# Kernel tuning notes

Hardware: AMD Instinct MI355X
Metric: run time of the kernel (lower is better)

The kernel has to match this reference:

```python
import jax, jax.numpy as jnp
import numpy as np

B, S, D, H, OPS = 1024, 512, 128, 128, 16
V2 = 64000  # vocabulary_size * 2


def _lstm_last(emb, lengths, W_ih, W_hh, b_ih, b_hh, h0, c0):
    # emb: [B, S, D]; returns hidden state at step lengths-1 for each sample: [B, H]
    bsz = emb.shape[0]
    x = jnp.swapaxes(emb, 0, 1)  # [S, B, D]
    h = jnp.broadcast_to(h0[0], (bsz, h0.shape[-1]))  # learnable init state, expanded over batch
    c = jnp.broadcast_to(c0[0], (bsz, c0.shape[-1]))

    def step(carry, x_t):
        h, c = carry
        gates = x_t @ W_ih.T + b_ih + h @ W_hh.T + b_hh  # [B, 4H]
        i, f, g, o = jnp.split(gates, 4, axis=-1)  # torch LSTM gate order: i, f, g, o
        i = jax.nn.sigmoid(i); f = jax.nn.sigmoid(f)
        g = jnp.tanh(g); o = jax.nn.sigmoid(o)
        c = f * c + i * g
        h = o * jnp.tanh(c)
        return (h, c), h

    _, hs = jax.lax.scan(step, (h, c), x)  # hs: [S, B, H]
    t = jnp.maximum(lengths, 1) - 1  # last valid step per ragged sequence
    return hs[t, jnp.arange(bsz)]  # [B, H]


def setup_inputs() -> dict:
    key = jax.random.key(0)
    ks = jax.random.split(key, 12)
    sc = 0.05
    return {
        "tokens": jax.random.randint(ks[0], (B, S), 0, V2, dtype=jnp.int32),
        "lengths": jax.random.randint(ks[1], (B,), 1, S + 1, dtype=jnp.int32),
        "operator_onehot": jax.random.uniform(ks[2], (B, OPS), dtype=jnp.float32),
        "embedding": jax.random.normal(ks[3], (V2, D), dtype=jnp.float32) * sc,
        "W_ih": jax.random.normal(ks[4], (4 * H, D), dtype=jnp.float32) * sc,
        "W_hh": jax.random.normal(ks[5], (4 * H, H), dtype=jnp.float32) * sc,
        "b_ih": jax.random.normal(ks[6], (4 * H,), dtype=jnp.float32) * sc,
        "b_hh": jax.random.normal(ks[7], (4 * H,), dtype=jnp.float32) * sc,
        "h0": jnp.zeros((1, 1, H), dtype=jnp.float32),
        "c0": jnp.zeros((1, 1, H), dtype=jnp.float32),
        "lin_W": jax.random.normal(ks[8], (2, H + OPS), dtype=jnp.float32) * sc,
        "lin_b": jax.random.normal(ks[9], (2,), dtype=jnp.float32) * sc,
    }


def reference(tokens, lengths, operator_onehot, embedding, W_ih, W_hh, b_ih, b_hh, h0, c0, lin_W, lin_b):
    emb = jax.nn.relu(embedding[tokens])  # [B, S, D] embedding lookup + ReLU
    h_last = jax.nn.relu(_lstm_last(emb, lengths, W_ih, W_hh, b_ih, b_hh, h0, c0))  # [B, H]
    combined = jnp.concatenate([h_last, operator_onehot], axis=1)  # feature union
    return combined @ lin_W.T + lin_b  # [B, 2] logits (training mode: no sigmoid)
```

## Files before the change

### kernel.cpp

```cpp
#include <hip/hip_runtime.h>
#include <hip/hip_bf16.h>

#define NB    1024
#define SEQ   512
#define DIM   128
#define HID   128
#define NOPS  16
#define FEAT  144
#define BQ    4
#define AST   144
#define XST   578
#define TKST  (SEQ + 16)

typedef __bf16 bf16x8 __attribute__((ext_vector_type(8)));
typedef float  floatx4 __attribute__((ext_vector_type(4)));

__device__ __forceinline__ float gate_s(float aL, float aH, float ka) {
    const float kS = -1.4426950408889634f;
    const float arg = __builtin_fmaf(kS, aL, __builtin_fmaf(kS, aH, ka));
    return __builtin_amdgcn_rcpf(1.0f + __builtin_amdgcn_exp2f(arg));
}
__device__ __forceinline__ float gate_t(float aL, float aH, float ka) {
    const float kT = -2.8853900817779268f;
    const float arg = __builtin_fmaf(kT, aL, __builtin_fmaf(kT, aH, ka));
    return 2.0f * __builtin_amdgcn_rcpf(1.0f + __builtin_amdgcn_exp2f(arg)) - 1.0f;
}
__device__ __forceinline__ float tanh_c(float x) {
    const float kT = -2.8853900817779268f;
    return 2.0f * __builtin_amdgcn_rcpf(1.0f + __builtin_amdgcn_exp2f(kT * x)) - 1.0f;
}

__device__ __forceinline__ void block_sync_lds() {
    asm volatile("s_waitcnt lgkmcnt(0)\n\ts_barrier" ::: "memory");
}

__global__ __launch_bounds__(512, 2)
void lstm_fused(const int* __restrict__ tokens, const int* __restrict__ lengths,
                const float* __restrict__ onehot, const float* __restrict__ emb,
                const float* __restrict__ Wih, const float* __restrict__ Whh,
                const float* __restrict__ bih, const float* __restrict__ bhh,
                const float* __restrict__ h0, const float* __restrict__ c0,
                const float* __restrict__ linW, const float* __restrict__ linb,
                float* __restrict__ out)
{
    __shared__ __align__(16) __bf16 xbuf[8 * XST];
    __shared__ __align__(16) __bf16 hbuf[2 * BQ * AST];
    __shared__ __align__(16) float  hlbuf[BQ * HID];
    __shared__ __align__(16) int    tkbuf[BQ * TKST];

    const int tid  = threadIdx.x;
    const int wave = tid >> 6;
    const int lane = tid & 63;
    const int quad = lane >> 4;
    const int lrow = lane & 15;
    const int bid  = blockIdx.x;

    bf16x8 wfx[4][4], wfh[4][4];
#pragma unroll
    for (int gt = 0; gt < 4; ++gt) {
        const int g = gt * 128 + wave * 16 + lrow;
#pragma unroll
        for (int kt = 0; kt < 4; ++kt) {
            const float* sx = Wih + g * DIM + kt * 32 + quad * 8;
            const float* sh = Whh + g * HID + kt * 32 + quad * 8;
            float4 a = *(const float4*)(sx);
            float4 b = *(const float4*)(sx + 4);
            bf16x8 v;
            v[0] = (__bf16)a.x; v[1] = (__bf16)a.y; v[2] = (__bf16)a.z; v[3] = (__bf16)a.w;
            v[4] = (__bf16)b.x; v[5] = (__bf16)b.y; v[6] = (__bf16)b.z; v[7] = (__bf16)b.w;
            wfx[gt][kt] = v;
            a = *(const float4*)(sh);
            b = *(const float4*)(sh + 4);
            v[0] = (__bf16)a.x; v[1] = (__bf16)a.y; v[2] = (__bf16)a.z; v[3] = (__bf16)a.w;
            v[4] = (__bf16)b.x; v[5] = (__bf16)b.y; v[6] = (__bf16)b.z; v[7] = (__bf16)b.w;
            wfh[gt][kt] = v;
        }
    }

    const int uu = wave * 16 + lrow;
    const int bq = bid * BQ + quad;
    int lenq = lengths[bq]; if (lenq < 1) lenq = 1;
    const int tlast = lenq - 1;

    int Lmax = 0;
#pragma unroll
    for (int s2 = 0; s2 < BQ; ++s2) {
        int l2 = lengths[bid * BQ + s2]; if (l2 < 1) l2 = 1;
        Lmax = (l2 > Lmax) ? l2 : Lmax;
    }

    const float kS = -1.4426950408889634f;
    const float kT = -2.8853900817779268f;
    const float karg0 = kS * (bih[0 * 128 + uu] + bhh[0 * 128 + uu]);
    const float karg1 = kS * (bih[1 * 128 + uu] + bhh[1 * 128 + uu]);
    const float karg2 = kT * (bih[2 * 128 + uu] + bhh[2 * 128 + uu]);
    const float karg3 = kS * (bih[3 * 128 + uu] + bhh[3 * 128 + uu]);

    float c  = c0[uu];
    float hl = 0.0f;

    const int m  = tid >> 7;
    const int u  = tid & 127;
    const int bm = bid * BQ + m;
    const int sm = m * AST + u;

    {
        const int4 tv = *(const int4*)(tokens + (size_t)bm * SEQ + (tid & 127) * 4);
        *(int4*)(&tkbuf[m * TKST + (tid & 127) * 4]) = tv;
        if (tid < BQ * 16)
            tkbuf[(tid >> 4) * TKST + SEQ + (tid & 15)] = 0;
    }

    hbuf[sm] = (__bf16)h0[u];
    const int* tokm = tokens + (size_t)bm * SEQ;
#pragma unroll
    for (int k = 0; k < 8; ++k) {
        float ek = emb[(size_t)tokm[k] * DIM + u];
        xbuf[k * XST + sm] = (__bf16)fmaxf(ek, 0.0f);
    }
    float e0 = emb[(size_t)tokm[8]  * DIM + u];
    float e1 = emb[(size_t)tokm[9]  * DIM + u];
    float e2 = emb[(size_t)tokm[10] * DIM + u];
    float e3 = emb[(size_t)tokm[11] * DIM + u];
    int   tk = tokm[12];

#define EREG(OFF) ((OFF) == 0 ? e0 : (OFF) == 1 ? e1 : (OFF) == 2 ? e2 : e3)

    const int xfbase = (lrow & 3) * XST + (lrow >> 2) * AST + quad * 8;
    const __bf16* const xfp[2] = { &xbuf[xfbase], &xbuf[4 * XST + xfbase] };
    const int habase = (lrow >> 2) * AST + quad * 8;
    const __bf16* const hf[2] = { &hbuf[habase], &hbuf[BQ * AST + habase] };
    __bf16* const hw[2] = { &hbuf[quad * AST + uu], &hbuf[BQ * AST + quad * AST + uu] };
    __bf16* const xw = &xbuf[sm];

    __syncthreads();

    const floatx4 zc = {0.0f, 0.0f, 0.0f, 0.0f};

    floatx4 xga[4], xgb[4];
    {
        bf16x8 af_[4];
#pragma unroll
        for (int kt = 0; kt < 4; ++kt)
            af_[kt] = *(const bf16x8*)(xfp[0] + kt * 32);
#pragma unroll
        for (int gt = 0; gt < 4; ++gt)
            xga[gt] = __builtin_amdgcn_mfma_f32_16x16x32_bf16(af_[0], wfx[gt][0], zc, 0, 0, 0);
#pragma unroll
        for (int kt = 1; kt < 4; ++kt)
#pragma unroll
            for (int gt = 0; gt < 4; ++gt)
                xga[gt] = __builtin_amdgcn_mfma_f32_16x16x32_bf16(af_[kt], wfx[gt][kt], xga[gt], 0, 0, 0);
    }
    block_sync_lds();

#define STEP(G, OFF, XGC, XGN) do {                                                  \
        const int t  = ts + OFF;                                                     \
        bf16x8 ah0 = *(const bf16x8*)(hf[OFF & 1] + 0 * 32);                         \
        bf16x8 ah2 = *(const bf16x8*)(hf[OFF & 1] + 2 * 32);                         \
        bf16x8 ah1 = *(const bf16x8*)(hf[OFF & 1] + 1 * 32);                         \
        bf16x8 ah3 = *(const bf16x8*)(hf[OFF & 1] + 3 * 32);                         \
        bf16x8 ax_ = *(const bf16x8*)(xfp[1 - (G)] + (OFF) * 32);                    \
        if (t + 8 < SEQ)         \
            xw[(4 * (G) + (OFF)) * XST] = (__bf16)fmaxf(EREG(OFF), 0.0f);            \
        if (t + 12 < SEQ)                                    \
            EREG(OFF) = emb[(size_t)tk * DIM + u];                                   \
        tk = tkbuf[m * TKST + t + 13];                                               \
        floatx4 aL[4], aH[4];                                                        \
        _Pragma("unroll") for (int gt = 0; gt < 4; ++gt)                             \
            aL[gt] = __builtin_amdgcn_mfma_f32_16x16x32_bf16(ah0, wfh[gt][0], XGC[gt], 0, 0, 0); \
        _Pragma("unroll") for (int gt = 0; gt < 4; ++gt)                             \
            aH[gt] = __builtin_amdgcn_mfma_f32_16x16x32_bf16(ah2, wfh[gt][2], zc, 0, 0, 0); \
        _Pragma("unroll") for (int gt = 0; gt < 4; ++gt)                             \
            aL[gt] = __builtin_amdgcn_mfma_f32_16x16x32_bf16(ah1, wfh[gt][1], aL[gt], 0, 0, 0); \
        _Pragma("unroll") for (int gt = 0; gt < 4; ++gt)                             \
            aH[gt] = __builtin_amdgcn_mfma_f32_16x16x32_bf16(ah3, wfh[gt][3], aH[gt], 0, 0, 0); \
        if (OFF == 0) {                                                              \
            _Pragma("unroll") for (int gt = 0; gt < 4; ++gt)                         \
                XGN[gt] = __builtin_amdgcn_mfma_f32_16x16x32_bf16(ax_, wfx[gt][0], zc, 0, 0, 0); \
        } else {                                                                     \
            _Pragma("unroll") for (int gt = 0; gt < 4; ++gt)                         \
                XGN[gt] = __builtin_amdgcn_mfma_f32_16x16x32_bf16(ax_, wfx[gt][OFF], XGN[gt], 0, 0, 0); \
        }                                                                            \
        const float ii = gate_s(aL[0][OFF], aH[0][OFF], karg0);                      \
        const float ff = gate_s(aL[1][OFF], aH[1][OFF], karg1);                      \
        const float g2 = gate_t(aL[2][OFF], aH[2][OFF], karg2);                      \
        const float oo = gate_s(aL[3][OFF], aH[3][OFF], karg3);                      \
        c = ff * c + ii * g2;                                                        \
        const float h = oo * tanh_c(c);                                              \
        if (t == tlast) hl = fmaxf(h, 0.0f);                                         \
        *hw[1 - (OFF & 1)] = (__bf16)h;                                              \
        block_sync_lds();                                                            \
    } while (0)

    for (int ts8 = 0; ts8 < Lmax; ts8 += 8) {
        {
            const int ts = ts8;
            STEP(0, 0, xga, xgb); STEP(0, 1, xga, xgb);
            STEP(0, 2, xga, xgb); STEP(0, 3, xga, xgb);
        }
        {
            const int ts = ts8 + 4;
            STEP(1, 0, xgb, xga); STEP(1, 1, xgb, xga);
            STEP(1, 2, xgb, xga); STEP(1, 3, xgb, xga);
        }
    }
#undef STEP
#undef EREG

    hlbuf[quad * HID + uu] = hl;
    __syncthreads();
    if (tid < 2 * BQ) {
        const int mm = tid >> 1, kk = tid & 1;
        const int bb = bid * BQ + mm;
        float a2 = linb[kk];
        for (int q = 0; q < HID; ++q)
            a2 += hlbuf[mm * HID + q] * linW[kk * FEAT + q];
        for (int o = 0; o < NOPS; ++o)
            a2 += onehot[bb * NOPS + o] * linW[kk * FEAT + HID + o];
        out[bb * 2 + kk] = a2;
    }
}

extern "C" void kernel_launch(void* const* d_in, const int* in_sizes, int n_in,
                              void* d_out, int out_size, void* d_ws, size_t ws_size,
                              hipStream_t stream) {
    const int*   tokens  = (const int*)d_in[0];
    const int*   lengths = (const int*)d_in[1];
    const float* onehot  = (const float*)d_in[2];
    const float* emb     = (const float*)d_in[3];
    const float* Wih     = (const float*)d_in[4];
    const float* Whh     = (const float*)d_in[5];
    const float* bih     = (const float*)d_in[6];
    const float* bhh     = (const float*)d_in[7];
    const float* h0      = (const float*)d_in[8];
    const float* c0      = (const float*)d_in[9];
    const float* linW    = (const float*)d_in[10];
    const float* linb    = (const float*)d_in[11];
    float* out = (float*)d_out;
    (void)in_sizes; (void)n_in; (void)out_size; (void)d_ws; (void)ws_size;

    lstm_fused<<<dim3(NB / BQ), dim3(512), 0, stream>>>(
        tokens, lengths, onehot, emb, Wih, Whh, bih, bhh, h0, c0, linW, linb, out);
}
```

Before: 421.8 us.

## Halve block to 4 waves, each owning two hidden-unit column tiles

The block drops from 512 to 256 threads, so each wave handles 32 hidden units (two 16-column MFMA tiles) instead of 16. Each wave holds twice the weight fragments in registers. The split-K aL/aH accumulation becomes a single 4-deep chain per tile. The input projection for the next 4 steps is now computed in one batch at step 3, instead of being spread over the steps. The aim is cheaper per-step barriers with fewer waves and more MFMA work between syncs. In exchange, register pressure rises, occupancy falls (launch bounds 256,1), and the per-step dependency chain gets longer.

```diff
diff --git a/kernel.cpp b/kernel.cpp
--- a/kernel.cpp
+++ b/kernel.cpp
@@ -15,15 +15,13 @@
 typedef __bf16 bf16x8 __attribute__((ext_vector_type(8)));
 typedef float  floatx4 __attribute__((ext_vector_type(4)));
 
-__device__ __forceinline__ float gate_s(float aL, float aH, float ka) {
+__device__ __forceinline__ float sig_a(float a, float ka) {
     const float kS = -1.4426950408889634f;
-    const float arg = __builtin_fmaf(kS, aL, __builtin_fmaf(kS, aH, ka));
-    return __builtin_amdgcn_rcpf(1.0f + __builtin_amdgcn_exp2f(arg));
-}
-__device__ __forceinline__ float gate_t(float aL, float aH, float ka) {
+    return __builtin_amdgcn_rcpf(1.0f + __builtin_amdgcn_exp2f(__builtin_fmaf(kS, a, ka)));
+}
+__device__ __forceinline__ float tanh_a(float a, float ka) {
     const float kT = -2.8853900817779268f;
-    const float arg = __builtin_fmaf(kT, aL, __builtin_fmaf(kT, aH, ka));
-    return 2.0f * __builtin_amdgcn_rcpf(1.0f + __builtin_amdgcn_exp2f(arg)) - 1.0f;
+    return 2.0f * __builtin_amdgcn_rcpf(1.0f + __builtin_amdgcn_exp2f(__builtin_fmaf(kT, a, ka))) - 1.0f;
 }
 __device__ __forceinline__ float tanh_c(float x) {
     const float kT = -2.8853900817779268f;
@@ -34,7 +32,7 @@
     asm volatile("s_waitcnt lgkmcnt(0)\n\ts_barrier" ::: "memory");
 }
 
-__global__ __launch_bounds__(512, 2)
+__global__ __launch_bounds__(256, 1)
 void lstm_fused(const int* __restrict__ tokens, const int* __restrict__ lengths,
                 const float* __restrict__ onehot, const float* __restrict__ emb,
                 const float* __restrict__ Wih, const float* __restrict__ Whh,
@@ -55,31 +53,34 @@
     const int lrow = lane & 15;
     const int bid  = blockIdx.x;
 
-    bf16x8 wfx[4][4], wfh[4][4];
+    bf16x8 wfx[4][2][4], wfh[4][2][4];
 #pragma unroll
     for (int gt = 0; gt < 4; ++gt) {
-        const int g = gt * 128 + wave * 16 + lrow;
-#pragma unroll
-        for (int kt = 0; kt < 4; ++kt) {
-            const float* sx = Wih + g * DIM + kt * 32 + quad * 8;
-            const float* sh = Whh + g * HID + kt * 32 + quad * 8;
-            float4 a = *(const float4*)(sx);
-            float4 b = *(const float4*)(sx + 4);
-            bf16x8 v;
-            v[0] = (__bf16)a.x; v[1] = (__bf16)a.y; v[2] = (__bf16)a.z; v[3] = (__bf16)a.w;
-            v[4] = (__bf16)b.x; v[5] = (__bf16)b.y; v[6] = (__bf16)b.z; v[7] = (__bf16)b.w;
-            wfx[gt][kt] = v;
-            a = *(const float4*)(sh);
-            b = *(const float4*)(sh + 4);
-            v[0] = (__bf16)a.x; v[1] = (__bf16)a.y; v[2] = (__bf16)a.z; v[3] = (__bf16)a.w;
-            v[4] = (__bf16)b.x; v[5] = (__bf16)b.y; v[6] = (__bf16)b.z; v[7] = (__bf16)b.w;
-            wfh[gt][kt] = v;
+#pragma unroll
+        for (int ct = 0; ct < 2; ++ct) {
+            const int g = gt * 128 + wave * 32 + ct * 16 + lrow;
+#pragma unroll
+            for (int kt = 0; kt < 4; ++kt) {
+                const float* sx = Wih + g * DIM + kt * 32 + quad * 8;
+                const float* sh = Whh + g * HID + kt * 32 + quad * 8;
+                float4 a = *(const float4*)(sx);
+                float4 b = *(const float4*)(sx + 4);
+                bf16x8 v;
+                v[0] = (__bf16)a.x; v[1] = (__bf16)a.y; v[2] = (__bf16)a.z; v[3] = (__bf16)a.w;
+                v[4] = (__bf16)b.x; v[5] = (__bf16)b.y; v[6] = (__bf16)b.z; v[7] = (__bf16)b.w;
+                wfx[gt][ct][kt] = v;
+                a = *(const float4*)(sh);
+                b = *(const float4*)(sh + 4);
+                v[0] = (__bf16)a.x; v[1] = (__bf16)a.y; v[2] = (__bf16)a.z; v[3] = (__bf16)a.w;
+                v[4] = (__bf16)b.x; v[5] = (__bf16)b.y; v[6] = (__bf16)b.z; v[7] = (__bf16)b.w;
+                wfh[gt][ct][kt] = v;
+            }
         }
     }
 
-    const int uu = wave * 16 + lrow;
-    const int bq = bid * BQ + quad;
-    int lenq = lengths[bq]; if (lenq < 1) lenq = 1;
+    const int uA = wave * 32 + lrow;
+    const int uB = uA + 16;
+    int lenq = lengths[bid * BQ + quad]; if (lenq < 1) lenq = 1;
     const int tlast = lenq - 1;
 
     int Lmax = 0;
@@ -91,124 +92,140 @@
 
     const float kS = -1.4426950408889634f;
     const float kT = -2.8853900817779268f;
-    const float karg0 = kS * (bih[0 * 128 + uu] + bhh[0 * 128 + uu]);
-    const float karg1 = kS * (bih[1 * 128 + uu] + bhh[1 * 128 + uu]);
-    const float karg2 = kT * (bih[2 * 128 + uu] + bhh[2 * 128 + uu]);
-    const float karg3 = kS * (bih[3 * 128 + uu] + bhh[3 * 128 + uu]);
-
-    float c  = c0[uu];
-    float hl = 0.0f;
-
-    const int m  = tid >> 7;
-    const int u  = tid & 127;
-    const int bm = bid * BQ + m;
-    const int sm = m * AST + u;
+    const float kA0 = kS * (bih[0 * 128 + uA] + bhh[0 * 128 + uA]);
+    const float kA1 = kS * (bih[1 * 128 + uA] + bhh[1 * 128 + uA]);
+    const float kA2 = kT * (bih[2 * 128 + uA] + bhh[2 * 128 + uA]);
+    const float kA3 = kS * (bih[3 * 128 + uA] + bhh[3 * 128 + uA]);
+    const float kB0 = kS * (bih[0 * 128 + uB] + bhh[0 * 128 + uB]);
+    const float kB1 = kS * (bih[1 * 128 + uB] + bhh[1 * 128 + uB]);
+    const float kB2 = kT * (bih[2 * 128 + uB] + bhh[2 * 128 + uB]);
+    const float kB3 = kS * (bih[3 * 128 + uB] + bhh[3 * 128 + uB]);
+
+    float cA = c0[uA], cB = c0[uB];
+    float hlA = 0.0f, hlB = 0.0f;
+
+    const int bm = bid * BQ + wave;
+    const int* tokm = tokens + (size_t)bm * SEQ;
 
     {
-        const int4 tv = *(const int4*)(tokens + (size_t)bm * SEQ + (tid & 127) * 4);
-        *(int4*)(&tkbuf[m * TKST + (tid & 127) * 4]) = tv;
+        *(int4*)(&tkbuf[wave * TKST + lane * 8])     = *(const int4*)(tokm + lane * 8);
+        *(int4*)(&tkbuf[wave * TKST + lane * 8 + 4]) = *(const int4*)(tokm + lane * 8 + 4);
         if (tid < BQ * 16)
             tkbuf[(tid >> 4) * TKST + SEQ + (tid & 15)] = 0;
     }
 
-    hbuf[sm] = (__bf16)h0[u];
-    const int* tokm = tokens + (size_t)bm * SEQ;
+    hbuf[wave * AST + lane]      = (__bf16)h0[lane];
+    hbuf[wave * AST + lane + 64] = (__bf16)h0[lane + 64];
 #pragma unroll
     for (int k = 0; k < 8; ++k) {
-        float ek = emb[(size_t)tokm[k] * DIM + u];
-        xbuf[k * XST + sm] = (__bf16)fmaxf(ek, 0.0f);
-    }
-    float e0 = emb[(size_t)tokm[8]  * DIM + u];
-    float e1 = emb[(size_t)tokm[9]  * DIM + u];
-    float e2 = emb[(size_t)tokm[10] * DIM + u];
-    float e3 = emb[(size_t)tokm[11] * DIM + u];
-    int   tk = tokm[12];
-
-#define EREG(OFF) ((OFF) == 0 ? e0 : (OFF) == 1 ? e1 : (OFF) == 2 ? e2 : e3)
+        const size_t row = (size_t)tokm[k] * DIM;
+        xbuf[k * XST + wave * AST + lane]      = (__bf16)fmaxf(emb[row + lane], 0.0f);
+        xbuf[k * XST + wave * AST + lane + 64] = (__bf16)fmaxf(emb[row + lane + 64], 0.0f);
+    }
+    float eA0 = emb[(size_t)tokm[8]  * DIM + lane], eB0 = emb[(size_t)tokm[8]  * DIM + lane + 64];
+    float eA1 = emb[(size_t)tokm[9]  * DIM + lane], eB1 = emb[(size_t)tokm[9]  * DIM + lane + 64];
+    float eA2 = emb[(size_t)tokm[10] * DIM + lane], eB2 = emb[(size_t)tokm[10] * DIM + lane + 64];
+    float eA3 = emb[(size_t)tokm[11] * DIM + lane], eB3 = emb[(size_t)tokm[11] * DIM + lane + 64];
+    int   tk  = tokm[12];
+
+#define EA(OFF) ((OFF) == 0 ? eA0 : (OFF) == 1 ? eA1 : (OFF) == 2 ? eA2 : eA3)
+#define EB(OFF) ((OFF) == 0 ? eB0 : (OFF) == 1 ? eB1 : (OFF) == 2 ? eB2 : eB3)
 
     const int xfbase = (lrow & 3) * XST + (lrow >> 2) * AST + quad * 8;
     const __bf16* const xfp[2] = { &xbuf[xfbase], &xbuf[4 * XST + xfbase] };
     const int habase = (lrow >> 2) * AST + quad * 8;
     const __bf16* const hf[2] = { &hbuf[habase], &hbuf[BQ * AST + habase] };
-    __bf16* const hw[2] = { &hbuf[quad * AST + uu], &hbuf[BQ * AST + quad * AST + uu] };
-    __bf16* const xw = &xbuf[sm];
+    __bf16* const hwA[2] = { &hbuf[quad * AST + uA], &hbuf[BQ * AST + quad * AST + uA] };
+    __bf16* const hwB[2] = { &hbuf[quad * AST + uB], &hbuf[BQ * AST + quad * AST + uB] };
+    __bf16* const xwA = &xbuf[wave * AST + lane];
+    __bf16* const xwB = &xbuf[wave * AST + lane + 64];
 
     __syncthreads();
 
     const floatx4 zc = {0.0f, 0.0f, 0.0f, 0.0f};
 
-    floatx4 xga[4], xgb[4];
+    floatx4 xg[4][2];
     {
         bf16x8 af_[4];
 #pragma unroll
         for (int kt = 0; kt < 4; ++kt)
             af_[kt] = *(const bf16x8*)(xfp[0] + kt * 32);
 #pragma unroll
-        for (int gt = 0; gt < 4; ++gt)
-            xga[gt] = __builtin_amdgcn_mfma_f32_16x16x32_bf16(af_[0], wfx[gt][0], zc, 0, 0, 0);
-#pragma unroll
-        for (int kt = 1; kt < 4; ++kt)
+        for (int kt = 0; kt < 4; ++kt)
 #pragma unroll
             for (int gt = 0; gt < 4; ++gt)
-                xga[gt] = __builtin_amdgcn_mfma_f32_16x16x32_bf16(af_[kt], wfx[gt][kt], xga[gt], 0, 0, 0);
+#pragma unroll
+                for (int ct = 0; ct < 2; ++ct)
+                    xg[gt][ct] = __builtin_amdgcn_mfma_f32_16x16x32_bf16(
+                        af_[kt], wfx[gt][ct][kt], kt == 0 ? zc : xg[gt][ct], 0, 0, 0);
     }
     block_sync_lds();
 
-#define STEP(G, OFF, XGC, XGN) do {                                                  \
-        const int t  = ts + OFF;                                                     \
-        bf16x8 ah0 = *(const bf16x8*)(hf[OFF & 1] + 0 * 32);                         \
-        bf16x8 ah2 = *(const bf16x8*)(hf[OFF & 1] + 2 * 32);                         \
-        bf16x8 ah1 = *(const bf16x8*)(hf[OFF & 1] + 1 * 32);                         \
-        bf16x8 ah3 = *(const bf16x8*)(hf[OFF & 1] + 3 * 32);                         \
-        bf16x8 ax_ = *(const bf16x8*)(xfp[1 - (G)] + (OFF) * 32);                    \
-        if (t + 8 < SEQ)         \
-            xw[(4 * (G) + (OFF)) * XST] = (__bf16)fmaxf(EREG(OFF), 0.0f);            \
-        if (t + 12 < SEQ)                                    \
-            EREG(OFF) = emb[(size_t)tk * DIM + u];                                   \
-        tk = tkbuf[m * TKST + t + 13];                                               \
-        floatx4 aL[4], aH[4];                                                        \
-        _Pragma("unroll") for (int gt = 0; gt < 4; ++gt)                             \
-            aL[gt] = __builtin_amdgcn_mfma_f32_16x16x32_bf16(ah0, wfh[gt][0], XGC[gt], 0, 0, 0); \
-        _Pragma("unroll") for (int gt = 0; gt < 4; ++gt)                             \
-            aH[gt] = __builtin_amdgcn_mfma_f32_16x16x32_bf16(ah2, wfh[gt][2], zc, 0, 0, 0); \
-        _Pragma("unroll") for (int gt = 0; gt < 4; ++gt)                             \
-            aL[gt] = __builtin_amdgcn_mfma_f32_16x16x32_bf16(ah1, wfh[gt][1], aL[gt], 0, 0, 0); \
-        _Pragma("unroll") for (int gt = 0; gt < 4; ++gt)                             \
-            aH[gt] = __builtin_amdgcn_mfma_f32_16x16x32_bf16(ah3, wfh[gt][3], aH[gt], 0, 0, 0); \
-        if (OFF == 0) {                                                              \
+#define STEP(G, OFF) do {                                                            \
+        const int t = ts + OFF;                                                      \
+        bf16x8 ah_[4];                                                               \
+        _Pragma("unroll") for (int kt = 0; kt < 4; ++kt)                             \
+            ah_[kt] = *(const bf16x8*)(hf[OFF & 1] + kt * 32);                       \
+        if (t + 8 < SEQ) {                \
+            xwA[(4 * (G) + (OFF)) * XST] = (__bf16)fmaxf(EA(OFF), 0.0f);             \
+            xwB[(4 * (G) + (OFF)) * XST] = (__bf16)fmaxf(EB(OFF), 0.0f);             \
+        }                                                                            \
+        if (t + 12 < SEQ) {                                  \
+            const size_t row = (size_t)tk * DIM;                                     \
+            EA(OFF) = emb[row + lane];                                               \
+            EB(OFF) = emb[row + lane + 64];                                          \
+        }                                                                            \
+        tk = tkbuf[wave * TKST + t + 13];                                            \
+        floatx4 acc[4][2];                                                           \
+        _Pragma("unroll") for (int kt = 0; kt < 4; ++kt)                             \
             _Pragma("unroll") for (int gt = 0; gt < 4; ++gt)                         \
-                XGN[gt] = __builtin_amdgcn_mfma_f32_16x16x32_bf16(ax_, wfx[gt][0], zc, 0, 0, 0); \
-        } else {                                                                     \
-            _Pragma("unroll") for (int gt = 0; gt < 4; ++gt)                         \
-                XGN[gt] = __builtin_amdgcn_mfma_f32_16x16x32_bf16(ax_, wfx[gt][OFF], XGN[gt], 0, 0, 0); \
+                _Pragma("unroll") for (int ct = 0; ct < 2; ++ct)                     \
+                    acc[gt][ct] = __builtin_amdgcn_mfma_f32_16x16x32_bf16(           \
+                        ah_[kt], wfh[gt][ct][kt], kt == 0 ? xg[gt][ct] : acc[gt][ct], 0, 0, 0); \
+        if (OFF == 3 && ts + 4 < Lmax) {              \
+            bf16x8 af_[4];                                                           \
+            _Pragma("unroll") for (int kt = 0; kt < 4; ++kt)                         \
+                af_[kt] = *(const bf16x8*)(xfp[1 - (G)] + kt * 32);                  \
+            _Pragma("unroll") for (int kt = 0; kt < 4; ++kt)                         \
+                _Pragma("unroll") for (int gt = 0; gt < 4; ++gt)                     \
+                    _Pragma("unroll") for (int ct = 0; ct < 2; ++ct)                 \
+                        xg[gt][ct] = __builtin_amdgcn_mfma_f32_16x16x32_bf16(        \
+                            af_[kt], wfx[gt][ct][kt], kt == 0 ? zc : xg[gt][ct], 0, 0, 0); \
         }                                                                            \
-        const float ii = gate_s(aL[0][OFF], aH[0][OFF], karg0);                      \
-        const float ff = gate_s(aL[1][OFF], aH[1][OFF], karg1);                      \
-        const float g2 = gate_t(aL[2][OFF], aH[2][OFF], karg2);                      \
-        const float oo = gate_s(aL[3][OFF], aH[3][OFF], karg3);                      \
-        c = ff * c + ii * g2;                                                        \
-        const float h = oo * tanh_c(c);                                              \
-        if (t == tlast) hl = fmaxf(h, 0.0f);                                         \
-        *hw[1 - (OFF & 1)] = (__bf16)h;                                              \
+        const float iA = sig_a (acc[0][0][OFF], kA0);                                \
+        const float fA = sig_a (acc[1][0][OFF], kA1);                                \
+        const float gA = tanh_a(acc[2][0][OFF], kA2);                                \
+        const float oA = sig_a (acc[3][0][OFF], kA3);                                \
+        const float iB = sig_a (acc[0][1][OFF], kB0);                                \
+        const float fB = sig_a (acc[1][1][OFF], kB1);                                \
+        const float gB = tanh_a(acc[2][1][OFF], kB2);                                \
+        const float oB = sig_a (acc[3][1][OFF], kB3);                                \
+        cA = fA * cA + iA * gA;                                                      \
+        cB = fB * cB + iB * gB;                                                      \
+        const float hA = oA * tanh_c(cA);                                            \
+        const float hB = oB * tanh_c(cB);                                            \
+        if (t == tlast) { hlA = fmaxf(hA, 0.0f); hlB = fmaxf(hB, 0.0f); }            \
+        *hwA[1 - (OFF & 1)] = (__bf16)hA;                                            \
+        *hwB[1 - (OFF & 1)] = (__bf16)hB;                                            \
         block_sync_lds();                                                            \
     } while (0)
 
     for (int ts8 = 0; ts8 < Lmax; ts8 += 8) {
         {
             const int ts = ts8;
-            STEP(0, 0, xga, xgb); STEP(0, 1, xga, xgb);
-            STEP(0, 2, xga, xgb); STEP(0, 3, xga, xgb);
+            STEP(0, 0); STEP(0, 1); STEP(0, 2); STEP(0, 3);
         }
         {
             const int ts = ts8 + 4;
-            STEP(1, 0, xgb, xga); STEP(1, 1, xgb, xga);
-            STEP(1, 2, xgb, xga); STEP(1, 3, xgb, xga);
+            STEP(1, 0); STEP(1, 1); STEP(1, 2); STEP(1, 3);
         }
     }
 #undef STEP
-#undef EREG
-
-    hlbuf[quad * HID + uu] = hl;
+#undef EA
+#undef EB
+
+    hlbuf[quad * HID + uA] = hlA;
+    hlbuf[quad * HID + uB] = hlB;
     __syncthreads();
     if (tid < 2 * BQ) {
         const int mm = tid >> 1, kk = tid & 1;
@@ -240,6 +257,6 @@
     float* out = (float*)d_out;
     (void)in_sizes; (void)n_in; (void)out_size; (void)d_ws; (void)ws_size;
 
-    lstm_fused<<<dim3(NB / BQ), dim3(512), 0, stream>>>(
+    lstm_fused<<<dim3(NB / BQ), dim3(256), 0, stream>>>(
         tokens, lengths, onehot, emb, Wih, Whh, bih, bhh, h0, c0, linW, linb, out);
 }
```

After: 459.2 us. 8.9% more time.
